# Optimization experiments

Measured on AMD Instinct MI355X. Metric: run time of the kernel, lower is better.

## Reference

```python
import jax, jax.numpy as jnp
import numpy as np

B, S, D = 2, 2048, 2048
NH, NKV = 16, 4
HD = D // NH          # 128
Q_DIM = NH * HD       # 2048
KV_DIM = NKV * HD     # 512
N_REP = NH // NKV     # 4


def setup_inputs() -> dict:
    key = jax.random.key(0)
    k1, k2, k3, k4 = jax.random.split(key, 4)
    x = jax.random.normal(k1, (B, S, D), dtype=jnp.float32)
    freqs_cis = jax.random.normal(k2, (S, HD), dtype=jnp.float32)
    Wqkv = jax.random.normal(k3, (Q_DIM + 2 * KV_DIM, D), dtype=jnp.float32) * (D ** -0.5)
    Wo = jax.random.normal(k4, (D, Q_DIM), dtype=jnp.float32) * (Q_DIM ** -0.5)
    return {"x": x, "freqs_cis": freqs_cis, "Wqkv": Wqkv, "Wo": Wo}


def _apply_rope(xq, xk, freqs_cis):
    # xq: [B,S,NH,HD], xk: [B,S,NKV,HD], freqs_cis: [S,HD] viewed as [S,1,HD//2,2]
    f = freqs_cis.reshape(S, 1, HD // 2, 2)
    f0, f1 = f[..., 0], f[..., 1]  # broadcast over batch & heads

    def rot(t):
        shp = t.shape
        tp = t.reshape(*shp[:-1], HD // 2, 2)
        t0, t1 = tp[..., 0], tp[..., 1]
        # row1 = <x, (f0,f1)>;  row0 = <x, (f1,-f0)>  (matches torch flip+negate)
        row1 = t0 * f0 + t1 * f1
        row0 = t0 * f1 - t1 * f0
        return jnp.stack([row0, row1], axis=-1).reshape(shp)

    return rot(xq), rot(xk)


def reference(x, freqs_cis, Wqkv, Wo):
    # Fused QKV projection (exact path: all RLA sketch dims = 0)
    xqkv = jnp.einsum('bsd,od->bso', x, Wqkv)
    xq = xqkv[..., :Q_DIM].reshape(B, S, NH, HD)
    xk = xqkv[..., Q_DIM:Q_DIM + KV_DIM].reshape(B, S, NKV, HD)
    xv = xqkv[..., Q_DIM + KV_DIM:].reshape(B, S, NKV, HD)

    xq, xk = _apply_rope(xq, xk, freqs_cis)

    # [B,H,S,HD]
    xq = xq.transpose(0, 2, 1, 3)
    xk = xk.transpose(0, 2, 1, 3)
    xv = xv.transpose(0, 2, 1, 3)

    # GQA: repeat kv heads n_rep times
    xk = jnp.repeat(xk, N_REP, axis=1)
    xv = jnp.repeat(xv, N_REP, axis=1)

    scale = 1.0 / jnp.sqrt(jnp.asarray(HD, dtype=xq.dtype))
    scores = jnp.einsum('bhqd,bhkd->bhqk', xq, xk) * scale
    causal = jnp.tril(jnp.ones((S, S), dtype=bool))
    scores = jnp.where(causal, scores, jnp.finfo(scores.dtype).min)
    probs = jax.nn.softmax(scores, axis=-1)
    out = jnp.einsum('bhqk,bhkd->bhqd', probs, xv)  # [B,H,S,HD]

    out = out.transpose(0, 2, 1, 3).reshape(B, S, Q_DIM)
    return jnp.einsum('bsq,dq->bsd', out, Wo)
```

## Files before the change

### kernel.cpp

```cpp
#include <hip/hip_runtime.h>
#include <hip/hip_bf16.h>
#include <cstdint>
#include <cstddef>

#define B_ 2
#define S_ 2048
#define NH_ 16
#define NKV_ 4
#define HD_ 128
#define QDIM_ 2048
#define KVDIM_ 512
#define QKV_ 3072

typedef __attribute__((ext_vector_type(8))) short short8;
typedef __attribute__((ext_vector_type(4))) short bhalf4;
typedef __attribute__((ext_vector_type(4))) float float4v;
typedef __attribute__((ext_vector_type(2))) float float2v;

__device__ __forceinline__ float bf2f(short u) {
  union { unsigned int i; float f; } v;
  v.i = ((unsigned int)(unsigned short)u) << 16;
  return v.f;
}
__device__ __forceinline__ short f2bf(float f) {
  union { float f; unsigned int i; } v; v.f = f;
  unsigned int x = v.i;
  x += 0x7fffu + ((x >> 16) & 1u);
  return (short)(x >> 16);
}

#if __has_builtin(__builtin_amdgcn_exp2f)
__device__ __forceinline__ float exp2fast(float x) { return __builtin_amdgcn_exp2f(x); }
#else
__device__ __forceinline__ float exp2fast(float x) { return exp2f(x); }
#endif

__device__ __forceinline__ unsigned int cvt_pk_bf16(float a, float b) {
  unsigned int r;
  asm("v_cvt_pk_bf16_f32 %0, %1, %2" : "=v"(r) : "v"(a), "v"(b));
  return r;
}

__device__ __forceinline__ void async_copy16(void* lds, const void* g) {
  __builtin_amdgcn_global_load_lds(
      (const __attribute__((address_space(1))) void*)g,
      (__attribute__((address_space(3))) void*)lds, 16, 0, 0);
}

__global__ void f32_to_bf16(const float* __restrict__ src, short* __restrict__ dst,
                            int n8) {
  int id = blockIdx.x * 256 + threadIdx.x;
  if (id >= n8) return;
  const float* f = src + (size_t)id * 8;
  float4v a = *(const float4v*)(f);
  float4v b = *(const float4v*)(f + 4);
  short8 r;
#pragma unroll
  for (int e = 0; e < 4; ++e) { r[e] = f2bf(a[e]); r[4 + e] = f2bf(b[e]); }
  *(short8*)(dst + (size_t)id * 8) = r;
}

template <int N, int K, bool CF32>
__global__ __launch_bounds__(256)
void gemm_nt_bf16(const short* __restrict__ A, const short* __restrict__ Bm,
                  void* __restrict__ Cp) {
  __shared__ __align__(16) short sA[128 * 32];
  __shared__ __align__(16) short sB[128 * 32];
  const int tid = threadIdx.x;
  const int m0 = blockIdx.y * 128, n0 = blockIdx.x * 128;
  const int wave = tid >> 6, lane = tid & 63;
  const int wm = (wave & 1) << 6, wn = (wave >> 1) << 6;
  const int lm = lane & 15, kg = lane >> 4;

  float4v acc[4][4];
#pragma unroll
  for (int i = 0; i < 4; ++i)
#pragma unroll
    for (int j = 0; j < 4; ++j)
      acc[i][j] = (float4v){0.f, 0.f, 0.f, 0.f};

  const int r0 = tid >> 2, c0 = tid & 3;
  const short* gA0 = A + (size_t)(m0 + r0) * K + c0 * 8;
  const short* gA1 = gA0 + (size_t)64 * K;
  const short* gB0 = Bm + (size_t)(n0 + r0) * K + c0 * 8;
  const short* gB1 = gB0 + (size_t)64 * K;
  short* lA0 = sA + tid * 8;
  short* lA1 = sA + 2048 + tid * 8;
  short* lB0 = sB + tid * 8;
  short* lB1 = sB + 2048 + tid * 8;

  for (int k0 = 0; k0 < K; k0 += 32) {
    async_copy16(lA0, gA0 + k0);
    async_copy16(lA1, gA1 + k0);
    async_copy16(lB0, gB0 + k0);
    async_copy16(lB1, gB1 + k0);
    __syncthreads();

    short8 a[4], b[4];
#pragma unroll
    for (int i = 0; i < 4; ++i)
      a[i] = *(const short8*)(sA + (wm + i * 16 + lm) * 32 + kg * 8);
#pragma unroll
    for (int j = 0; j < 4; ++j)
      b[j] = *(const short8*)(sB + (wn + j * 16 + lm) * 32 + kg * 8);
#pragma unroll
    for (int i = 0; i < 4; ++i)
#pragma unroll
      for (int j = 0; j < 4; ++j)
        acc[i][j] = __builtin_amdgcn_mfma_f32_16x16x32_bf16(a[i], b[j], acc[i][j], 0, 0, 0);
    __syncthreads();
  }

#pragma unroll
  for (int i = 0; i < 4; ++i) {
    const int rb = m0 + wm + i * 16 + kg * 4;
#pragma unroll
    for (int j = 0; j < 4; ++j) {
      const int cc = n0 + wn + j * 16 + lm;
#pragma unroll
      for (int r = 0; r < 4; ++r) {
        if constexpr (CF32)
          ((float*)Cp)[(size_t)(rb + r) * N + cc] = acc[i][j][r];
        else
          ((short*)Cp)[(size_t)(rb + r) * N + cc] = f2bf(acc[i][j][r]);
      }
    }
  }
}

__global__ __launch_bounds__(256)
void gemm_qkv_rope(const short* __restrict__ A, const short* __restrict__ Bm,
                   const float* __restrict__ freqs, short* __restrict__ Qr,
                   short* __restrict__ Kr, short* __restrict__ Vv) {
  constexpr int K = 2048;
  __shared__ __align__(16) short sA[128 * 32];
  __shared__ __align__(16) short sB[128 * 32];
  const int tid = threadIdx.x;
  const int m0 = blockIdx.y * 128, n0 = blockIdx.x * 128;
  const int wave = tid >> 6, lane = tid & 63;
  const int wm = (wave & 1) << 6, wn = (wave >> 1) << 6;
  const int lm = lane & 15, kg = lane >> 4;

  float4v acc[4][4];
#pragma unroll
  for (int i = 0; i < 4; ++i)
#pragma unroll
    for (int j = 0; j < 4; ++j)
      acc[i][j] = (float4v){0.f, 0.f, 0.f, 0.f};

  const int r0 = tid >> 2, c0 = tid & 3;
  const short* gA0 = A + (size_t)(m0 + r0) * K + c0 * 8;
  const short* gA1 = gA0 + (size_t)64 * K;
  const short* gB0 = Bm + (size_t)(n0 + r0) * K + c0 * 8;
  const short* gB1 = gB0 + (size_t)64 * K;
  short* lA0 = sA + tid * 8;
  short* lA1 = sA + 2048 + tid * 8;
  short* lB0 = sB + tid * 8;
  short* lB1 = sB + 2048 + tid * 8;

  for (int k0 = 0; k0 < K; k0 += 32) {
    async_copy16(lA0, gA0 + k0);
    async_copy16(lA1, gA1 + k0);
    async_copy16(lB0, gB0 + k0);
    async_copy16(lB1, gB1 + k0);
    __syncthreads();

    short8 a[4], b[4];
#pragma unroll
    for (int i = 0; i < 4; ++i)
      a[i] = *(const short8*)(sA + (wm + i * 16 + lm) * 32 + kg * 8);
#pragma unroll
    for (int j = 0; j < 4; ++j)
      b[j] = *(const short8*)(sB + (wn + j * 16 + lm) * 32 + kg * 8);
#pragma unroll
    for (int i = 0; i < 4; ++i)
#pragma unroll
      for (int j = 0; j < 4; ++j)
        acc[i][j] = __builtin_amdgcn_mfma_f32_16x16x32_bf16(a[i], b[j], acc[i][j], 0, 0, 0);
    __syncthreads();
  }

  const float SCQ = 0.12751744543795287f;
#pragma unroll
  for (int i = 0; i < 4; ++i) {
    const int rb = m0 + wm + i * 16 + kg * 4;
#pragma unroll
    for (int j = 0; j < 4; ++j) {
      const int cc = n0 + wn + j * 16 + lm;
#pragma unroll
      for (int r = 0; r < 4; ++r) {
        const int token = rb + r;
        const int s = token & (S_ - 1), bq = token >> 11;
        float v = acc[i][j][r];
        if (cc < QDIM_ + KVDIM_) {
          float p = __shfl_xor(v, 1, 64);
          int d; short* dst; float sc;
          if (cc < QDIM_) {
            const int hh = cc >> 7; d = cc & 127;
            dst = Qr + ((size_t)(bq * NH_ + hh) * S_ + s) * HD_ + d;
            sc = SCQ;
          } else {
            const int cv = cc - QDIM_;
            const int hh = cv >> 7; d = cv & 127;
            dst = Kr + ((size_t)(bq * NKV_ + hh) * S_ + s) * HD_ + d;
            sc = 1.f;
          }
          float2v f = *(const float2v*)(freqs + (size_t)s * HD_ + (d & ~1));
          const float t0 = (d & 1) ? p : v, t1 = (d & 1) ? v : p;
          const float out = (d & 1) ? (t0 * f[0] + t1 * f[1])
                                    : (t0 * f[1] - t1 * f[0]);
          *dst = f2bf(out * sc);
        } else {
          const int cv = cc - QDIM_ - KVDIM_;
          const int hh = cv >> 7, d = cv & 127;
          Kr[0] = Kr[0];
          Vv[((size_t)(bq * NKV_ + hh) * S_ + s) * HD_ + d] = f2bf(v);
        }
      }
    }
  }
}

__global__ void transpose_v(const short* __restrict__ Vv, short* __restrict__ Vt) {
  __shared__ short t[64][72];
  const int s0 = blockIdx.x * 64, d0 = blockIdx.y * 64;
  const short* src = Vv + (size_t)blockIdx.z * S_ * HD_;
  short* dst = Vt + (size_t)blockIdx.z * S_ * HD_;
  const int tid = threadIdx.x;
#pragma unroll
  for (int c = 0; c < 2; ++c) {
    int ch = tid + 256 * c;
    int row = ch >> 3, kc = ch & 7;
    *(short8*)(&t[row][kc * 8]) =
        *(const short8*)(src + (size_t)(s0 + row) * HD_ + d0 + kc * 8);
  }
  __syncthreads();
#pragma unroll
  for (int c = 0; c < 2; ++c) {
    int ch = tid + 256 * c;
    int drow = ch >> 3, sc = ch & 7;
    short8 w;
#pragma unroll
    for (int j = 0; j < 8; ++j) w[j] = t[sc * 8 + j][drow];
    *(short8*)(dst + (size_t)(d0 + drow) * S_ + s0 + sc * 8) = w;
  }
}

#define TK 128

__global__ __launch_bounds__(256, 2)
void attn_causal(const short* __restrict__ Q, const short* __restrict__ K,
                 const short* __restrict__ Vt, short* __restrict__ O) {
  const int bh = blockIdx.x;
  const int qt = 31 - (int)blockIdx.y;
  const int b = bh >> 4, h = bh & 15;
  const int kvh = h >> 2;
  const int tid = threadIdx.x, wave = tid >> 6, lane = tid & 63;
  const int lm = lane & 15, kg = lane >> 4;

  __shared__ __align__(16) short sK[TK * HD_];
  __shared__ __align__(16) short sVt[HD_ * TK];

  const short* Qb = Q + (size_t)(b * NH_ + h) * S_ * HD_;
  const short* Kb = K + (size_t)(b * NKV_ + kvh) * S_ * HD_;
  const short* Vtb = Vt + (size_t)(b * NKV_ + kvh) * S_ * HD_;

  auto stageK = [&](int k0) {
#pragma unroll
    for (int c = 0; c < 8; ++c) {
      int ch = tid + 256 * c;
      int row = ch >> 4, kc = ch & 15;
      async_copy16(sK + ch * 8,
                   Kb + (size_t)(k0 + row) * HD_ + (kc ^ (row & 7)) * 8);
    }
  };
  auto stageV = [&](int k0) {
#pragma unroll
    for (int c = 0; c < 8; ++c) {
      int ch = tid + 256 * c;
      int row = ch >> 4, kc = ch & 15;
      async_copy16(sVt + ch * 8,
                   Vtb + (size_t)row * S_ + k0 + (kc ^ (row & 7)) * 8);
    }
  };

  const int qglob = qt * 64 + wave * 16 + lm;
  short8 qf[4];
#pragma unroll
  for (int kk = 0; kk < 4; ++kk)
    qf[kk] = *(const short8*)(Qb + (size_t)qglob * HD_ + kk * 32 + kg * 8);

  float mcur = -1e9f, lcur = 0.f;
  float4v o[8];
#pragma unroll
  for (int df = 0; df < 8; ++df) o[df] = (float4v){0.f, 0.f, 0.f, 0.f};

  stageK(0);
  const int nst = (qt + 2) >> 1;
  for (int s = 0; s < nst; ++s) {
    const int k0 = s * TK;
    const bool last = (s == nst - 1);

    __syncthreads();
    stageV(k0);

    float4v sfT[8];
#pragma unroll
    for (int mj = 0; mj < 8; ++mj) sfT[mj] = (float4v){0.f, 0.f, 0.f, 0.f};
    __builtin_amdgcn_s_setprio(1);
#pragma unroll
    for (int kk = 0; kk < 4; ++kk) {
      int kd = kk * 4 + kg;
#pragma unroll
      for (int mj = 0; mj < 8; ++mj) {
        int row = mj * 16 + lm;
        short8 af = *(const short8*)(sK + row * HD_ + (kd ^ (row & 7)) * 8);
        sfT[mj] = __builtin_amdgcn_mfma_f32_16x16x32_bf16(af, qf[kk], sfT[mj], 0, 0, 0);
      }
    }
    __builtin_amdgcn_s_setprio(0);

    if (last) {
#pragma unroll
      for (int mj = 0; mj < 8; ++mj)
#pragma unroll
        for (int r = 0; r < 4; ++r) {
          int kcol = k0 + mj * 16 + kg * 4 + r;
          sfT[mj][r] = (kcol <= qglob) ? sfT[mj][r] : -3e38f;
        }
    }

    float mx = -3e38f;
#pragma unroll
    for (int mj = 0; mj < 8; ++mj)
#pragma unroll
      for (int r = 0; r < 4; ++r) mx = fmaxf(mx, sfT[mj][r]);
    mx = fmaxf(mx, __shfl_xor(mx, 16, 64));
    mx = fmaxf(mx, __shfl_xor(mx, 32, 64));
    const bool need = (mx > mcur + 4.f);
    const float mnew = fmaxf(mcur, mx);
    const float alpha = need ? exp2fast(mcur - mnew) : 1.f;
    const float m_use = need ? mnew : mcur;
    float rs = 0.f;
    bhalf4 pb[8];
#pragma unroll
    for (int t = 0; t < 8; ++t) {
      float e0 = exp2fast(sfT[t][0] - m_use);
      float e1 = exp2fast(sfT[t][1] - m_use);
      float e2 = exp2fast(sfT[t][2] - m_use);
      float e3 = exp2fast(sfT[t][3] - m_use);
      rs += (e0 + e1) + (e2 + e3);
      union { unsigned int u[2]; bhalf4 v; } pk;
      pk.u[0] = cvt_pk_bf16(e0, e1);
      pk.u[1] = cvt_pk_bf16(e2, e3);
      pb[t] = pk.v;
    }
    rs += __shfl_xor(rs, 16, 64);
    rs += __shfl_xor(rs, 32, 64);
    mcur = m_use;
    lcur = lcur * alpha + rs;

    __syncthreads();
    if (!last) stageK(k0 + TK);

    if (__any(need)) {
#pragma unroll
      for (int df = 0; df < 8; ++df)
#pragma unroll
        for (int r = 0; r < 4; ++r) o[df][r] *= alpha;
    }

    __builtin_amdgcn_s_setprio(1);
#pragma unroll
    for (int t = 0; t < 8; ++t) {
      int kc = t * 2 + (kg >> 1);
#pragma unroll
      for (int df = 0; df < 8; ++df) {
        int row = df * 16 + lm;
        bhalf4 va = *(const bhalf4*)(sVt + row * TK + (kc ^ (row & 7)) * 8 +
                                     (kg & 1) * 4);
        o[df] = __builtin_amdgcn_mfma_f32_16x16x16bf16_1k(va, pb[t], o[df], 0, 0, 0);
      }
    }
    __builtin_amdgcn_s_setprio(0);
  }

  const float inv = 1.f / lcur;
  const size_t rowoff = (size_t)(b * S_ + qglob) * QDIM_ + h * HD_ + kg * 4;
#pragma unroll
  for (int df = 0; df < 8; ++df) {
    bhalf4 w;
    w[0] = f2bf(o[df][0] * inv);
    w[1] = f2bf(o[df][1] * inv);
    w[2] = f2bf(o[df][2] * inv);
    w[3] = f2bf(o[df][3] * inv);
    *(bhalf4*)(O + rowoff + df * 16) = w;
  }
}

extern "C" void kernel_launch(void* const* d_in, const int* in_sizes, int n_in,
                              void* d_out, int out_size, void* d_ws, size_t ws_size,
                              hipStream_t stream) {
  const float* x     = (const float*)d_in[0];
  const float* freqs = (const float*)d_in[1];
  const float* Wqkv  = (const float*)d_in[2];
  const float* Wo    = (const float*)d_in[3];
  float* out = (float*)d_out;

  short* ws     = (short*)d_ws;
  short* xb     = ws;
  short* Wob    = ws;
  short* Wqkvb  = ws + (size_t)4096 * 2048;
  short* xqkv   = Wqkvb + (size_t)QKV_ * 2048;
  short* attn   = xqkv;
  short* Qr     = xqkv + (size_t)4096 * QKV_;
  short* Kr     = Qr + (size_t)B_ * NH_ * S_ * HD_;
  short* Vv     = Kr + (size_t)B_ * NKV_ * S_ * HD_;
  short* Vtg    = Vv + (size_t)B_ * NKV_ * S_ * HD_;

  f32_to_bf16<<<(4096 * 2048 / 8) / 256, 256, 0, stream>>>(x, xb, 4096 * 2048 / 8);
  f32_to_bf16<<<(QKV_ * 2048 / 8) / 256, 256, 0, stream>>>(Wqkv, Wqkvb, QKV_ * 2048 / 8);
  gemm_qkv_rope<<<dim3(QKV_ / 128, 4096 / 128), 256, 0, stream>>>(
      xb, Wqkvb, freqs, Qr, Kr, Vv);
  f32_to_bf16<<<(2048 * 2048 / 8) / 256, 256, 0, stream>>>(Wo, Wob, 2048 * 2048 / 8);
  transpose_v<<<dim3(S_ / 64, HD_ / 64, B_ * NKV_), 256, 0, stream>>>(Vv, Vtg);
  attn_causal<<<dim3(32, 32), 256, 0, stream>>>(Qr, Kr, Vtg, attn);
  gemm_nt_bf16<2048, 2048, true>
      <<<dim3(2048 / 128, 4096 / 128), 256, 0, stream>>>(attn, Wob, out);
}
```

Baseline: 329.2 us.

## Stage QKV GEMM epilogue through LDS and fuse V transpose into it

The QKV GEMM epilogue now writes RoPE-rotated Q/K tiles into a padded shared-memory buffer and then stores them to global memory as coalesced 16-byte vectors, replacing scattered 2-byte stores. For V tiles the epilogue writes a transposed layout into shared memory and emits V^T directly, which removes the separate transpose_v kernel along with its extra global read and write. The cost is a larger LDS allocation per block (about 34 KB), which may reduce occupancy, plus an added barrier.

```diff
diff --git a/kernel.cpp b/kernel.cpp
--- a/kernel.cpp
+++ b/kernel.cpp
@@ -131,10 +131,12 @@
 __global__ __launch_bounds__(256)
 void gemm_qkv_rope(const short* __restrict__ A, const short* __restrict__ Bm,
                    const float* __restrict__ freqs, short* __restrict__ Qr,
-                   short* __restrict__ Kr, short* __restrict__ Vv) {
+                   short* __restrict__ Kr, short* __restrict__ Vt) {
   constexpr int K = 2048;
-  __shared__ __align__(16) short sA[128 * 32];
-  __shared__ __align__(16) short sB[128 * 32];
+  constexpr int ROWP = 136;
+  __shared__ __align__(16) short smem[128 * ROWP];
+  short* sA = smem;
+  short* sB = smem + 4096;
   const int tid = threadIdx.x;
   const int m0 = blockIdx.y * 128, n0 = blockIdx.x * 128;
   const int wave = tid >> 6, lane = tid & 63;
@@ -180,69 +182,58 @@
     __syncthreads();
   }
 
-  const float SCQ = 0.12751744543795287f;
-#pragma unroll
-  for (int i = 0; i < 4; ++i) {
-    const int rb = m0 + wm + i * 16 + kg * 4;
-#pragma unroll
-    for (int j = 0; j < 4; ++j) {
-      const int cc = n0 + wn + j * 16 + lm;
-#pragma unroll
-      for (int r = 0; r < 4; ++r) {
-        const int token = rb + r;
-        const int s = token & (S_ - 1), bq = token >> 11;
-        float v = acc[i][j][r];
-        if (cc < QDIM_ + KVDIM_) {
-          float p = __shfl_xor(v, 1, 64);
-          int d; short* dst; float sc;
-          if (cc < QDIM_) {
-            const int hh = cc >> 7; d = cc & 127;
-            dst = Qr + ((size_t)(bq * NH_ + hh) * S_ + s) * HD_ + d;
-            sc = SCQ;
-          } else {
-            const int cv = cc - QDIM_;
-            const int hh = cv >> 7; d = cv & 127;
-            dst = Kr + ((size_t)(bq * NKV_ + hh) * S_ + s) * HD_ + d;
-            sc = 1.f;
-          }
-          float2v f = *(const float2v*)(freqs + (size_t)s * HD_ + (d & ~1));
-          const float t0 = (d & 1) ? p : v, t1 = (d & 1) ? v : p;
-          const float out = (d & 1) ? (t0 * f[0] + t1 * f[1])
-                                    : (t0 * f[1] - t1 * f[0]);
-          *dst = f2bf(out * sc);
-        } else {
-          const int cv = cc - QDIM_ - KVDIM_;
-          const int hh = cv >> 7, d = cv & 127;
-          Kr[0] = Kr[0];
-          Vv[((size_t)(bq * NKV_ + hh) * S_ + s) * HD_ + d] = f2bf(v);
+  const int nb = blockIdx.x;
+  const bool isV = (nb >= 20);
+  const int s0 = m0 & (S_ - 1);
+  const int bq = m0 >> 11;
+
+  if (!isV) {
+    const float sc = (nb < 16) ? 0.12751744543795287f : 1.f;
+#pragma unroll
+    for (int i = 0; i < 4; ++i) {
+#pragma unroll
+      for (int j = 0; j < 4; ++j) {
+        const int d = wn + j * 16 + lm;
+#pragma unroll
+        for (int r = 0; r < 4; ++r) {
+          const int trow = wm + i * 16 + kg * 4 + r;
+          const float v = acc[i][j][r];
+          const float p = __shfl_xor(v, 1, 64);
+          const float2v f =
+              *(const float2v*)(freqs + (size_t)(s0 + trow) * HD_ + (d & ~1));
+          const float outv = (d & 1) ? (p * f[0] + v * f[1])
+                                     : (v * f[1] - p * f[0]);
+          smem[trow * ROWP + d] = f2bf(outv * sc);
         }
       }
     }
-  }
-}
-
-__global__ void transpose_v(const short* __restrict__ Vv, short* __restrict__ Vt) {
-  __shared__ short t[64][72];
-  const int s0 = blockIdx.x * 64, d0 = blockIdx.y * 64;
-  const short* src = Vv + (size_t)blockIdx.z * S_ * HD_;
-  short* dst = Vt + (size_t)blockIdx.z * S_ * HD_;
-  const int tid = threadIdx.x;
-#pragma unroll
-  for (int c = 0; c < 2; ++c) {
-    int ch = tid + 256 * c;
-    int row = ch >> 3, kc = ch & 7;
-    *(short8*)(&t[row][kc * 8]) =
-        *(const short8*)(src + (size_t)(s0 + row) * HD_ + d0 + kc * 8);
-  }
-  __syncthreads();
-#pragma unroll
-  for (int c = 0; c < 2; ++c) {
-    int ch = tid + 256 * c;
-    int drow = ch >> 3, sc = ch & 7;
-    short8 w;
-#pragma unroll
-    for (int j = 0; j < 8; ++j) w[j] = t[sc * 8 + j][drow];
-    *(short8*)(dst + (size_t)(d0 + drow) * S_ + s0 + sc * 8) = w;
+    __syncthreads();
+    short* gout = (nb < 16)
+        ? Qr + ((size_t)(bq * NH_ + nb) * S_ + s0) * HD_
+        : Kr + ((size_t)(bq * NKV_ + (nb - 16)) * S_ + s0) * HD_;
+#pragma unroll
+    for (int it = 0; it < 8; ++it) {
+      const int ch = tid + 256 * it, row = ch >> 4, cn = ch & 15;
+      *(short8*)(gout + (size_t)row * HD_ + cn * 8) =
+          *(const short8*)(smem + row * ROWP + cn * 8);
+    }
+  } else {
+#pragma unroll
+    for (int i = 0; i < 4; ++i)
+#pragma unroll
+      for (int j = 0; j < 4; ++j)
+#pragma unroll
+        for (int r = 0; r < 4; ++r)
+          smem[(wn + j * 16 + lm) * ROWP + (wm + i * 16 + kg * 4 + r)] =
+              f2bf(acc[i][j][r]);
+    __syncthreads();
+    short* gv = Vt + (size_t)(bq * NKV_ + (nb - 20)) * HD_ * S_;
+#pragma unroll
+    for (int it = 0; it < 8; ++it) {
+      const int ch = tid + 256 * it, d = ch >> 4, cn = ch & 15;
+      *(short8*)(gv + (size_t)d * S_ + s0 + cn * 8) =
+          *(const short8*)(smem + d * ROWP + cn * 8);
+    }
   }
 }
 
@@ -411,19 +402,16 @@
   short* xb     = ws;
   short* Wob    = ws;
   short* Wqkvb  = ws + (size_t)4096 * 2048;
-  short* xqkv   = Wqkvb + (size_t)QKV_ * 2048;
-  short* attn   = xqkv;
-  short* Qr     = xqkv + (size_t)4096 * QKV_;
+  short* attn   = Wqkvb + (size_t)QKV_ * 2048;
+  short* Qr     = attn + (size_t)4096 * 2048;
   short* Kr     = Qr + (size_t)B_ * NH_ * S_ * HD_;
-  short* Vv     = Kr + (size_t)B_ * NKV_ * S_ * HD_;
-  short* Vtg    = Vv + (size_t)B_ * NKV_ * S_ * HD_;
+  short* Vtg    = Kr + (size_t)B_ * NKV_ * S_ * HD_;
 
   f32_to_bf16<<<(4096 * 2048 / 8) / 256, 256, 0, stream>>>(x, xb, 4096 * 2048 / 8);
   f32_to_bf16<<<(QKV_ * 2048 / 8) / 256, 256, 0, stream>>>(Wqkv, Wqkvb, QKV_ * 2048 / 8);
   gemm_qkv_rope<<<dim3(QKV_ / 128, 4096 / 128), 256, 0, stream>>>(
-      xb, Wqkvb, freqs, Qr, Kr, Vv);
+      xb, Wqkvb, freqs, Qr, Kr, Vtg);
   f32_to_bf16<<<(2048 * 2048 / 8) / 256, 256, 0, stream>>>(Wo, Wob, 2048 * 2048 / 8);
-  transpose_v<<<dim3(S_ / 64, HD_ / 64, B_ * NKV_), 256, 0, stream>>>(Vv, Vtg);
   attn_causal<<<dim3(32, 32), 256, 0, stream>>>(Qr, Kr, Vtg, attn);
   gemm_nt_bf16<2048, 2048, true>
       <<<dim3(2048 / 128, 4096 / 128), 256, 0, stream>>>(attn, Wob, out);
```

After: 332.4 us. No clear change (+1.0%).
